# Kernel tuning notes

Measured on AMD Instinct MI355X. Metric: run time of the kernel, lower is better.

Reference implementation:

```python
import jax, jax.numpy as jnp
import numpy as np

N, FIN, H, FOUT = 4096, 128, 4, 64
NEG_INF = -1e9


def _xavier(key, shape):
    fan_in, fan_out = shape[-2], shape[-1]
    limit = float(np.sqrt(6.0 / (fan_in + fan_out)))
    return jax.random.uniform(key, shape, jnp.float32, -limit, limit)


def setup_inputs() -> dict:
    key = jax.random.key(0)
    ks = jax.random.split(key, 7)
    x = jax.random.normal(ks[0], (N, FIN), jnp.float32)
    u = jax.random.uniform(ks[1], (N, N))
    mask = jnp.where(u < 0.02, 0.0, NEG_INF).astype(jnp.float32)
    idx = jnp.arange(N)
    mask = mask.at[idx, idx].set(0.0)
    proj_param = _xavier(ks[2], (H, FIN, FOUT))          # per-head projection
    score_src = _xavier(ks[3], (H, FOUT, 1))             # scoring_fn_source (IMP1 layout)
    score_tgt = _xavier(ks[4], (H, FOUT, 1))             # scoring_fn_target
    skip_w = _xavier(ks[5], (H * FOUT, FIN))             # skip_proj Linear weight
    bias = jnp.zeros((H * FOUT,), jnp.float32)
    return {"x": x, "mask": mask, "proj_param": proj_param,
            "score_src": score_src, "score_tgt": score_tgt,
            "skip_w": skip_w, "bias": bias}


def reference(x, mask, proj_param, score_src, score_tgt, skip_w, bias):
    # project: [1,N,Fin] @ [H,Fin,Fout] -> [H,N,Fout]
    h = jnp.einsum('nf,hfo->hno', x, proj_param)
    # additive (Bahdanau-style) scores
    s_src = jnp.matmul(h, score_src)                     # [H,N,1]
    s_tgt = jnp.matmul(h, score_tgt)                     # [H,N,1]
    all_scores = jax.nn.leaky_relu(s_src + jnp.swapaxes(s_tgt, 1, 2), 0.2)  # [H,N,N]
    attn = jax.nn.softmax(all_scores + mask[None, :, :], axis=-1)           # [H,N,N]
    # aggregate: [H,N,N] @ [H,N,Fout] -> [N,H,Fout]
    out = jnp.einsum('hnm,hmo->nho', attn, h)
    # skip connection (dims differ: Fin != H*Fout -> use skip_proj)
    out = out + jnp.matmul(x, skip_w.T).reshape(N, H, FOUT)
    out = out.reshape(N, H * FOUT) + bias                # concat heads + bias
    return jax.nn.elu(out)
```

## Files before the change

kernel.cpp:

```cpp
#include <hip/hip_runtime.h>
#include <hip/hip_bf16.h>
#include <math.h>


#define NN   4096
#define FIN  128
#define NH   4
#define FO   64
#define HF   256
#define LIST 192
#define GEMM_BLOCKS 512
#define ROWS_PER 2

typedef unsigned short ushort_t;
typedef unsigned int uint4n __attribute__((ext_vector_type(4)));

__device__ __forceinline__ ushort_t f2bf(float f) {
    __hip_bfloat16 h = __float2bfloat16(f);
    union { __hip_bfloat16 h; ushort_t u; } c; c.h = h; return c.u;
}
__device__ __forceinline__ float bf2f(ushort_t u) {
    union { unsigned int i; float f; } c; c.i = ((unsigned int)u) << 16; return c.f;
}

__global__ __launch_bounds__(256) void k0_gemm(
        const float* __restrict__ x,
        const float* __restrict__ proj,
        const float* __restrict__ skw,
        const float* __restrict__ asrc,
        const float* __restrict__ atgt,
        ushort_t* __restrict__ h2b, float* __restrict__ skip_ws,
        float* __restrict__ src4, float* __restrict__ tgt4) {
    __shared__ float sA[64 * 68];
    __shared__ float sB[64 * 64];
    const int tid = threadIdx.x;
    const int blk = blockIdx.x;

    const int bc = blk >> 6;
    const int i0 = (blk & 63) * 64;
    const int tx = tid & 15, ty = tid >> 4;
    const int r0 = ty << 2, c0 = tx << 2;
    float acc[4][4] = {};

    #pragma unroll
    for (int kb = 0; kb < FIN; kb += 64) {
        if (kb) __syncthreads();
        #pragma unroll
        for (int q = 0; q < 4; q++) {
            int s   = tid + q * 256;
            int row = s >> 4;
            int c4  = (s & 15) << 2;
            float4 v = *(const float4*)(x + (size_t)(i0 + row) * FIN + kb + c4);
            float* d = sA + row * 68 + c4;
            d[0] = v.x; d[1] = v.y; d[2] = v.z; d[3] = v.w;
        }
        if (bc < 4) {
            const float4* src = (const float4*)(proj + (size_t)bc * FIN * FO
                                                + (size_t)kb * FO);
            #pragma unroll
            for (int q = 0; q < 4; q++) {
                int s = tid + q * 256;
                *(float4*)(sB + (size_t)s * 4) = src[s];
            }
        } else {
            const float* sw = skw + (size_t)(bc - 4) * 64 * FIN;
            #pragma unroll
            for (int q = 0; q < 4; q++) {
                int s  = tid + q * 256;
                int c  = s & 63;
                int k4 = (s >> 6) << 2;
                float4 v = *(const float4*)(sw + (size_t)c * FIN + kb + k4);
                sB[(k4 + 0) * 64 + c] = v.x;
                sB[(k4 + 1) * 64 + c] = v.y;
                sB[(k4 + 2) * 64 + c] = v.z;
                sB[(k4 + 3) * 64 + c] = v.w;
            }
        }
        __syncthreads();

        #pragma unroll 2
        for (int k = 0; k < 64; k += 4) {
            alignas(16) float a[4][4];
            alignas(16) float b[4][4];
            #pragma unroll
            for (int rr = 0; rr < 4; rr++)
                *(float4*)a[rr] = *(const float4*)(sA + (r0 + rr) * 68 + k);
            #pragma unroll
            for (int kk = 0; kk < 4; kk++)
                *(float4*)b[kk] = *(const float4*)(sB + (k + kk) * 64 + c0);
            #pragma unroll
            for (int kk = 0; kk < 4; kk++)
                #pragma unroll
                for (int rr = 0; rr < 4; rr++)
                    #pragma unroll
                    for (int cc = 0; cc < 4; cc++)
                        acc[rr][cc] = fmaf(a[rr][kk], b[kk][cc], acc[rr][cc]);
        }
    }

    if (bc < 4) {
        #pragma unroll
        for (int rr = 0; rr < 4; rr++) {
            ushort4 hv;
            hv.x = f2bf(acc[rr][0]); hv.y = f2bf(acc[rr][1]);
            hv.z = f2bf(acc[rr][2]); hv.w = f2bf(acc[rr][3]);
            *(ushort4*)(h2b + (size_t)(i0 + r0 + rr) * HF + bc * 64 + c0) = hv;
        }
        float as[4], at[4];
        #pragma unroll
        for (int cc = 0; cc < 4; cc++) {
            as[cc] = asrc[bc * FO + c0 + cc];
            at[cc] = atgt[bc * FO + c0 + cc];
        }
        #pragma unroll
        for (int rr = 0; rr < 4; rr++) {
            float ps = acc[rr][0] * as[0] + acc[rr][1] * as[1]
                     + acc[rr][2] * as[2] + acc[rr][3] * as[3];
            float pt = acc[rr][0] * at[0] + acc[rr][1] * at[1]
                     + acc[rr][2] * at[2] + acc[rr][3] * at[3];
            #pragma unroll
            for (int off = 8; off >= 1; off >>= 1) {
                ps += __shfl_xor(ps, off, 64);
                pt += __shfl_xor(pt, off, 64);
            }
            if (tx == 0) {
                int i = i0 + r0 + rr;
                src4[(size_t)i * 4 + bc] = ps;
                tgt4[(size_t)i * 4 + bc] = pt;
            }
        }
    } else {
        float* dst = skip_ws + (size_t)i0 * HF + (bc - 4) * 64;
        #pragma unroll
        for (int rr = 0; rr < 4; rr++)
            *(float4*)(dst + (size_t)(r0 + rr) * HF + c0) = *(float4*)acc[rr];
    }
}

struct K1Shared {
    int   s_j[LIST];
    float s_p[4][LIST + 1];
    float s_red[4][256];
    int   s_cnt[4];
    float s_inv[4];
};

__device__ __forceinline__ void k1_row(
        K1Shared* sh, unsigned hm, float sc, float skipv, float bv, int i,
        int tid, int lane, int w,
        const ushort_t* __restrict__ h2b,
        const float* __restrict__ tgt4,
        float* __restrict__ out) {
    const int cl = __popc(hm);
    int incl = cl;
    #pragma unroll
    for (int o = 1; o < 64; o <<= 1) {
        int t = __shfl_up(incl, o, 64);
        if (lane >= o) incl += t;
    }
    const int excl = incl - cl;
    if (lane == 63) sh->s_cnt[w] = incl;
    __syncthreads();
    const int t0 = sh->s_cnt[0], t1 = sh->s_cnt[1],
              t2 = sh->s_cnt[2], t3 = sh->s_cnt[3];
    const int off = (w > 0 ? t0 : 0) + (w > 1 ? t1 : 0) + (w > 2 ? t2 : 0);
    int c = t0 + t1 + t2 + t3;
    c = c < LIST ? c : LIST;

    int p = off + excl;
    unsigned mm = hm;
    while (mm) {
        int b = __builtin_ctz(mm);
        mm &= mm - 1;
        if (p < LIST)
            sh->s_j[p] = (w << 10) + ((b >> 2) << 8) + (lane << 2) + (b & 3);
        p++;
    }
    __syncthreads();

    float lsum = 0.f;
    for (int kk = lane; kk < c; kk += 64) {
        int j = sh->s_j[kk];
        float pv = sc + tgt4[(size_t)j * 4 + w];
        pv = pv > 0.f ? pv : 0.2f * pv;
        pv = __expf(pv);
        sh->s_p[w][kk] = pv;
        lsum += pv;
    }
    #pragma unroll
    for (int o = 32; o >= 1; o >>= 1)
        lsum += __shfl_xor(lsum, o, 64);
    if (lane == 0) sh->s_inv[w] = lsum > 0.f ? 1.0f / lsum : 0.0f;
    __syncthreads();

    const int h = lane >> 4;
    const ushort_t* hp = h2b + 4 * lane;
    float4 acc = {0.f, 0.f, 0.f, 0.f};
    int kk = w;
    for (; kk + 12 < c; kk += 16) {
        int   j0 = sh->s_j[kk],      j1 = sh->s_j[kk + 4];
        int   j2 = sh->s_j[kk + 8],  j3 = sh->s_j[kk + 12];
        float p0 = sh->s_p[h][kk],   p1 = sh->s_p[h][kk + 4];
        float p2 = sh->s_p[h][kk + 8], p3 = sh->s_p[h][kk + 12];
        ushort4 a0 = *(const ushort4*)(hp + (size_t)j0 * HF);
        ushort4 a1 = *(const ushort4*)(hp + (size_t)j1 * HF);
        ushort4 a2 = *(const ushort4*)(hp + (size_t)j2 * HF);
        ushort4 a3 = *(const ushort4*)(hp + (size_t)j3 * HF);
        acc.x = fmaf(p0, bf2f(a0.x), acc.x);
        acc.y = fmaf(p0, bf2f(a0.y), acc.y);
        acc.z = fmaf(p0, bf2f(a0.z), acc.z);
        acc.w = fmaf(p0, bf2f(a0.w), acc.w);
        acc.x = fmaf(p1, bf2f(a1.x), acc.x);
        acc.y = fmaf(p1, bf2f(a1.y), acc.y);
        acc.z = fmaf(p1, bf2f(a1.z), acc.z);
        acc.w = fmaf(p1, bf2f(a1.w), acc.w);
        acc.x = fmaf(p2, bf2f(a2.x), acc.x);
        acc.y = fmaf(p2, bf2f(a2.y), acc.y);
        acc.z = fmaf(p2, bf2f(a2.z), acc.z);
        acc.w = fmaf(p2, bf2f(a2.w), acc.w);
        acc.x = fmaf(p3, bf2f(a3.x), acc.x);
        acc.y = fmaf(p3, bf2f(a3.y), acc.y);
        acc.z = fmaf(p3, bf2f(a3.z), acc.z);
        acc.w = fmaf(p3, bf2f(a3.w), acc.w);
    }
    for (; kk < c; kk += 4) {
        int   j0 = sh->s_j[kk];
        float p0 = sh->s_p[h][kk];
        ushort4 a0 = *(const ushort4*)(hp + (size_t)j0 * HF);
        acc.x = fmaf(p0, bf2f(a0.x), acc.x);
        acc.y = fmaf(p0, bf2f(a0.y), acc.y);
        acc.z = fmaf(p0, bf2f(a0.z), acc.z);
        acc.w = fmaf(p0, bf2f(a0.w), acc.w);
    }
    *(float4*)&sh->s_red[w][4 * lane] = acc;
    __syncthreads();

    float tot = sh->s_red[0][tid] + sh->s_red[1][tid]
              + sh->s_red[2][tid] + sh->s_red[3][tid];
    float vv = tot * sh->s_inv[tid >> 6] + skipv + bv;
    vv = vv > 0.f ? vv : expm1f(vv);
    out[(size_t)i * HF + tid] = vv;
}

__global__ __launch_bounds__(256) void k1_attn(
        const unsigned int* __restrict__ mask,
        const ushort_t* __restrict__ h2b,
        const float* __restrict__ skip_ws,
        const float* __restrict__ src4,
        const float* __restrict__ tgt4,
        const float* __restrict__ bias,
        float* __restrict__ out) {
    __shared__ K1Shared sh;
    const int tid  = threadIdx.x;
    const int lane = tid & 63, w = tid >> 6;
    const int i0   = blockIdx.x * ROWS_PER;

    const uint4n* mb = (const uint4n*)mask;
    const size_t base = (size_t)i0 * 1024 + (size_t)(w * 256 + lane);
    uint4n m0[4];
    #pragma unroll
    for (int s = 0; s < 4; s++) m0[s] = mb[base + s * 64];

    const float skip0 = skip_ws[(size_t)i0 * HF + tid];
    const float skip1 = skip_ws[(size_t)(i0 + 1) * HF + tid];
    const float bv    = bias[tid];
    const float sc0   = src4[(size_t)i0 * 4 + w];
    const float sc1   = src4[(size_t)(i0 + 1) * 4 + w];

    unsigned hm0 = 0;
    #pragma unroll
    for (int s = 0; s < 4; s++)
        #pragma unroll
        for (int e = 0; e < 4; e++)
            hm0 |= ((m0[s][e] & 0x7fffffffu) == 0u ? 1u : 0u) << (s * 4 + e);

    uint4n m1[4];
    #pragma unroll
    for (int s = 0; s < 4; s++) m1[s] = mb[base + 1024 + s * 64];

    k1_row(&sh, hm0, sc0, skip0, bv, i0, tid, lane, w, h2b, tgt4, out);
    __syncthreads();

    unsigned hm1 = 0;
    #pragma unroll
    for (int s = 0; s < 4; s++)
        #pragma unroll
        for (int e = 0; e < 4; e++)
            hm1 |= ((m1[s][e] & 0x7fffffffu) == 0u ? 1u : 0u) << (s * 4 + e);

    k1_row(&sh, hm1, sc1, skip1, bv, i0 + 1, tid, lane, w, h2b, tgt4, out);
}

extern "C" void kernel_launch(void* const* d_in, const int* in_sizes, int n_in,
                              void* d_out, int out_size, void* d_ws, size_t ws_size,
                              hipStream_t stream) {
    const float*        x    = (const float*)d_in[0];
    const unsigned int* mask = (const unsigned int*)d_in[1];
    const float*        proj = (const float*)d_in[2];
    const float*        asrc = (const float*)d_in[3];
    const float*        atgt = (const float*)d_in[4];
    const float*        skw  = (const float*)d_in[5];
    const float*        bias = (const float*)d_in[6];
    float*              out  = (float*)d_out;

    char* ws = (char*)d_ws;
    ushort_t* h2b     = (ushort_t*)ws;
    float*    skip_ws = (float*)(ws + (2u << 20));
    float*    src4    = (float*)(ws + (6u << 20));
    float*    tgt4    = (float*)(ws + (6u << 20) + (64u << 10));

    hipLaunchKernelGGL(k0_gemm, dim3(GEMM_BLOCKS), dim3(256), 0, stream,
                       x, proj, skw, asrc, atgt,
                       h2b, skip_ws, src4, tgt4);
    hipLaunchKernelGGL(k1_attn, dim3(NN / ROWS_PER), dim3(256), 0, stream,
                       mask, h2b, skip_ws, src4, tgt4, bias, out);
}
```

Measured before the change: 128.7 us.

## Assign one wavefront per attention row and drop block-level synchronisation

Result: no change. 127.7 us (-0.8%).

```diff
diff --git a/kernel.cpp b/kernel.cpp
--- a/kernel.cpp
+++ b/kernel.cpp
@@ -10,7 +10,6 @@
 #define HF   256
 #define LIST 192
 #define GEMM_BLOCKS 512
-#define ROWS_PER 2
 
 typedef unsigned short ushort_t;
 typedef unsigned int uint4n __attribute__((ext_vector_type(4)));
@@ -137,21 +136,40 @@
     }
 }
 
-struct K1Shared {
-    int   s_j[LIST];
-    float s_p[4][LIST + 1];
-    float s_red[4][256];
-    int   s_cnt[4];
-    float s_inv[4];
-};
-
-__device__ __forceinline__ void k1_row(
-        K1Shared* sh, unsigned hm, float sc, float skipv, float bv, int i,
-        int tid, int lane, int w,
+__global__ __launch_bounds__(256, 4) void k1_attn(
+        const unsigned int* __restrict__ mask,
         const ushort_t* __restrict__ h2b,
+        const float* __restrict__ skip_ws,
+        const float* __restrict__ src4,
         const float* __restrict__ tgt4,
+        const float* __restrict__ bias,
         float* __restrict__ out) {
-    const int cl = __popc(hm);
+    __shared__ ushort_t s_j[4][LIST];
+    __shared__ uint2    s_rec[4][4][LIST + 1];
+    const int tid  = threadIdx.x;
+    const int lane = tid & 63, w = tid >> 6;
+    const int i    = blockIdx.x * 4 + w;
+    const int h    = lane >> 4;
+    const int g    = lane & 15;
+
+    const uint4n* mb = (const uint4n*)(mask + (size_t)i * NN);
+    uint4n m[16];
+    #pragma unroll
+    for (int s = 0; s < 16; s++) m[s] = mb[s * 64 + lane];
+
+    const float4 skipv = *(const float4*)(skip_ws + (size_t)i * HF + 4 * lane);
+    const float4 bv    = *(const float4*)(bias + 4 * lane);
+    const float  sc    = src4[(size_t)i * 4 + h];
+
+    unsigned long long hm = 0ull;
+    #pragma unroll
+    for (int s = 0; s < 16; s++)
+        #pragma unroll
+        for (int e = 0; e < 4; e++)
+            if ((m[s][e] & 0x7fffffffu) == 0u)
+                hm |= 1ull << (s * 4 + e);
+
+    const int cl = __popcll(hm);
     int incl = cl;
     #pragma unroll
     for (int o = 1; o < 64; o <<= 1) {
@@ -159,53 +177,52 @@
         if (lane >= o) incl += t;
     }
     const int excl = incl - cl;
-    if (lane == 63) sh->s_cnt[w] = incl;
-    __syncthreads();
-    const int t0 = sh->s_cnt[0], t1 = sh->s_cnt[1],
-              t2 = sh->s_cnt[2], t3 = sh->s_cnt[3];
-    const int off = (w > 0 ? t0 : 0) + (w > 1 ? t1 : 0) + (w > 2 ? t2 : 0);
-    int c = t0 + t1 + t2 + t3;
+    int c = __shfl(incl, 63, 64);
     c = c < LIST ? c : LIST;
 
-    int p = off + excl;
-    unsigned mm = hm;
-    while (mm) {
-        int b = __builtin_ctz(mm);
-        mm &= mm - 1;
-        if (p < LIST)
-            sh->s_j[p] = (w << 10) + ((b >> 2) << 8) + (lane << 2) + (b & 3);
-        p++;
-    }
-    __syncthreads();
+    {
+        int p = excl;
+        unsigned long long mm = hm;
+        while (mm) {
+            int b = __builtin_ctzll(mm);
+            mm &= mm - 1;
+            if (p < LIST)
+                s_j[w][p] = (ushort_t)((b >> 2) * 256 + lane * 4 + (b & 3));
+            p++;
+        }
+    }
 
     float lsum = 0.f;
-    for (int kk = lane; kk < c; kk += 64) {
-        int j = sh->s_j[kk];
-        float pv = sc + tgt4[(size_t)j * 4 + w];
+    for (int kk = g; kk < c; kk += 16) {
+        int j = s_j[w][kk];
+        float pv = sc + tgt4[(size_t)j * 4 + h];
         pv = pv > 0.f ? pv : 0.2f * pv;
         pv = __expf(pv);
-        sh->s_p[w][kk] = pv;
+        uint2 r;
+        r.x = __float_as_uint(pv);
+        r.y = (unsigned)j << 9;
+        s_rec[w][h][kk] = r;
         lsum += pv;
     }
     #pragma unroll
-    for (int o = 32; o >= 1; o >>= 1)
+    for (int o = 8; o >= 1; o >>= 1)
         lsum += __shfl_xor(lsum, o, 64);
-    if (lane == 0) sh->s_inv[w] = lsum > 0.f ? 1.0f / lsum : 0.0f;
-    __syncthreads();
-
-    const int h = lane >> 4;
-    const ushort_t* hp = h2b + 4 * lane;
+    const float inv = lsum > 0.f ? 1.0f / lsum : 0.0f;
+
+    const char* hp = (const char*)(h2b + 4 * lane);
     float4 acc = {0.f, 0.f, 0.f, 0.f};
-    int kk = w;
-    for (; kk + 12 < c; kk += 16) {
-        int   j0 = sh->s_j[kk],      j1 = sh->s_j[kk + 4];
-        int   j2 = sh->s_j[kk + 8],  j3 = sh->s_j[kk + 12];
-        float p0 = sh->s_p[h][kk],   p1 = sh->s_p[h][kk + 4];
-        float p2 = sh->s_p[h][kk + 8], p3 = sh->s_p[h][kk + 12];
-        ushort4 a0 = *(const ushort4*)(hp + (size_t)j0 * HF);
-        ushort4 a1 = *(const ushort4*)(hp + (size_t)j1 * HF);
-        ushort4 a2 = *(const ushort4*)(hp + (size_t)j2 * HF);
-        ushort4 a3 = *(const ushort4*)(hp + (size_t)j3 * HF);
+    int kk = 0;
+    for (; kk + 3 < c; kk += 4) {
+        uint2 r0 = s_rec[w][h][kk + 0];
+        uint2 r1 = s_rec[w][h][kk + 1];
+        uint2 r2 = s_rec[w][h][kk + 2];
+        uint2 r3 = s_rec[w][h][kk + 3];
+        ushort4 a0 = *(const ushort4*)(hp + r0.y);
+        ushort4 a1 = *(const ushort4*)(hp + r1.y);
+        ushort4 a2 = *(const ushort4*)(hp + r2.y);
+        ushort4 a3 = *(const ushort4*)(hp + r3.y);
+        float p0 = __uint_as_float(r0.x), p1 = __uint_as_float(r1.x);
+        float p2 = __uint_as_float(r2.x), p3 = __uint_as_float(r3.x);
         acc.x = fmaf(p0, bf2f(a0.x), acc.x);
         acc.y = fmaf(p0, bf2f(a0.y), acc.y);
         acc.z = fmaf(p0, bf2f(a0.z), acc.z);
@@ -223,72 +240,26 @@
         acc.z = fmaf(p3, bf2f(a3.z), acc.z);
         acc.w = fmaf(p3, bf2f(a3.w), acc.w);
     }
-    for (; kk < c; kk += 4) {
-        int   j0 = sh->s_j[kk];
-        float p0 = sh->s_p[h][kk];
-        ushort4 a0 = *(const ushort4*)(hp + (size_t)j0 * HF);
+    for (; kk < c; kk++) {
+        uint2 r0 = s_rec[w][h][kk];
+        ushort4 a0 = *(const ushort4*)(hp + r0.y);
+        float p0 = __uint_as_float(r0.x);
         acc.x = fmaf(p0, bf2f(a0.x), acc.x);
         acc.y = fmaf(p0, bf2f(a0.y), acc.y);
         acc.z = fmaf(p0, bf2f(a0.z), acc.z);
         acc.w = fmaf(p0, bf2f(a0.w), acc.w);
     }
-    *(float4*)&sh->s_red[w][4 * lane] = acc;
-    __syncthreads();
-
-    float tot = sh->s_red[0][tid] + sh->s_red[1][tid]
-              + sh->s_red[2][tid] + sh->s_red[3][tid];
-    float vv = tot * sh->s_inv[tid >> 6] + skipv + bv;
-    vv = vv > 0.f ? vv : expm1f(vv);
-    out[(size_t)i * HF + tid] = vv;
-}
-
-__global__ __launch_bounds__(256) void k1_attn(
-        const unsigned int* __restrict__ mask,
-        const ushort_t* __restrict__ h2b,
-        const float* __restrict__ skip_ws,
-        const float* __restrict__ src4,
-        const float* __restrict__ tgt4,
-        const float* __restrict__ bias,
-        float* __restrict__ out) {
-    __shared__ K1Shared sh;
-    const int tid  = threadIdx.x;
-    const int lane = tid & 63, w = tid >> 6;
-    const int i0   = blockIdx.x * ROWS_PER;
-
-    const uint4n* mb = (const uint4n*)mask;
-    const size_t base = (size_t)i0 * 1024 + (size_t)(w * 256 + lane);
-    uint4n m0[4];
-    #pragma unroll
-    for (int s = 0; s < 4; s++) m0[s] = mb[base + s * 64];
-
-    const float skip0 = skip_ws[(size_t)i0 * HF + tid];
-    const float skip1 = skip_ws[(size_t)(i0 + 1) * HF + tid];
-    const float bv    = bias[tid];
-    const float sc0   = src4[(size_t)i0 * 4 + w];
-    const float sc1   = src4[(size_t)(i0 + 1) * 4 + w];
-
-    unsigned hm0 = 0;
-    #pragma unroll
-    for (int s = 0; s < 4; s++)
-        #pragma unroll
-        for (int e = 0; e < 4; e++)
-            hm0 |= ((m0[s][e] & 0x7fffffffu) == 0u ? 1u : 0u) << (s * 4 + e);
-
-    uint4n m1[4];
-    #pragma unroll
-    for (int s = 0; s < 4; s++) m1[s] = mb[base + 1024 + s * 64];
-
-    k1_row(&sh, hm0, sc0, skip0, bv, i0, tid, lane, w, h2b, tgt4, out);
-    __syncthreads();
-
-    unsigned hm1 = 0;
-    #pragma unroll
-    for (int s = 0; s < 4; s++)
-        #pragma unroll
-        for (int e = 0; e < 4; e++)
-            hm1 |= ((m1[s][e] & 0x7fffffffu) == 0u ? 1u : 0u) << (s * 4 + e);
-
-    k1_row(&sh, hm1, sc1, skip1, bv, i0 + 1, tid, lane, w, h2b, tgt4, out);
+
+    float4 vv;
+    vv.x = acc.x * inv + skipv.x + bv.x;
+    vv.y = acc.y * inv + skipv.y + bv.y;
+    vv.z = acc.z * inv + skipv.z + bv.z;
+    vv.w = acc.w * inv + skipv.w + bv.w;
+    vv.x = vv.x > 0.f ? vv.x : expm1f(vv.x);
+    vv.y = vv.y > 0.f ? vv.y : expm1f(vv.y);
+    vv.z = vv.z > 0.f ? vv.z : expm1f(vv.z);
+    vv.w = vv.w > 0.f ? vv.w : expm1f(vv.w);
+    *(float4*)(out + (size_t)i * HF + 4 * lane) = vv;
 }
 
 extern "C" void kernel_launch(void* const* d_in, const int* in_sizes, int n_in,
@@ -312,6 +283,6 @@
     hipLaunchKernelGGL(k0_gemm, dim3(GEMM_BLOCKS), dim3(256), 0, stream,
                        x, proj, skw, asrc, atgt,
                        h2b, skip_ws, src4, tgt4);
-    hipLaunchKernelGGL(k1_attn, dim3(NN / ROWS_PER), dim3(256), 0, stream,
+    hipLaunchKernelGGL(k1_attn, dim3(NN / 4), dim3(256), 0, stream,
                        mask, h2b, skip_ws, src4, tgt4, bias, out);
 }
```

## Split mask scan into a separate bitmask kernel ahead of attention

Applied to the files above, without the earlier changes.

Measured after the change: 130.1 us. Within noise of the previous version (+1.0%).

```diff
diff --git a/kernel.cpp b/kernel.cpp
--- a/kernel.cpp
+++ b/kernel.cpp
@@ -10,7 +10,6 @@
 #define HF   256
 #define LIST 192
 #define GEMM_BLOCKS 512
-#define ROWS_PER 2
 
 typedef unsigned short ushort_t;
 typedef unsigned int uint4n __attribute__((ext_vector_type(4)));
@@ -137,7 +136,32 @@
     }
 }
 
-struct K1Shared {
+__global__ __launch_bounds__(256) void k_scan(
+        const unsigned int* __restrict__ mask,
+        ushort_t* __restrict__ bm) {
+    const int lane = threadIdx.x & 63, w = threadIdx.x >> 6;
+    const int wid  = blockIdx.x * 4 + w;
+    const uint4n* mb = (const uint4n*)mask;
+
+    #pragma unroll
+    for (int rep = 0; rep < 2; rep++) {
+        const int sg  = wid + rep * 8192;
+        const int row = sg >> 2, seg = sg & 3;
+        const uint4n* p = mb + (size_t)row * 1024 + seg * 256 + lane * 4;
+        uint4n v0 = p[0], v1 = p[1], v2 = p[2], v3 = p[3];
+        unsigned hm = 0;
+        #pragma unroll
+        for (int e = 0; e < 4; e++) {
+            hm |= ((v0[e] & 0x7fffffffu) == 0u ? 1u : 0u) << (0 * 4 + e);
+            hm |= ((v1[e] & 0x7fffffffu) == 0u ? 1u : 0u) << (1 * 4 + e);
+            hm |= ((v2[e] & 0x7fffffffu) == 0u ? 1u : 0u) << (2 * 4 + e);
+            hm |= ((v3[e] & 0x7fffffffu) == 0u ? 1u : 0u) << (3 * 4 + e);
+        }
+        bm[(size_t)row * 256 + seg * 64 + lane] = (ushort_t)hm;
+    }
+}
+
+struct K2Shared {
     int   s_j[LIST];
     float s_p[4][LIST + 1];
     float s_red[4][256];
@@ -145,12 +169,24 @@
     float s_inv[4];
 };
 
-__device__ __forceinline__ void k1_row(
-        K1Shared* sh, unsigned hm, float sc, float skipv, float bv, int i,
-        int tid, int lane, int w,
+__global__ __launch_bounds__(256) void k2_attn(
+        const ushort_t* __restrict__ bm,
         const ushort_t* __restrict__ h2b,
+        const float* __restrict__ skip_ws,
+        const float* __restrict__ src4,
         const float* __restrict__ tgt4,
+        const float* __restrict__ bias,
         float* __restrict__ out) {
+    __shared__ K2Shared sh;
+    const int tid  = threadIdx.x;
+    const int lane = tid & 63, w = tid >> 6;
+    const int i    = blockIdx.x;
+
+    const unsigned hm = bm[(size_t)i * 256 + w * 64 + lane];
+    const float skipv = skip_ws[(size_t)i * HF + tid];
+    const float bv    = bias[tid];
+    const float sc    = src4[(size_t)i * 4 + w];
+
     const int cl = __popc(hm);
     int incl = cl;
     #pragma unroll
@@ -159,38 +195,39 @@
         if (lane >= o) incl += t;
     }
     const int excl = incl - cl;
-    if (lane == 63) sh->s_cnt[w] = incl;
+    if (lane == 63) sh.s_cnt[w] = incl;
     __syncthreads();
-    const int t0 = sh->s_cnt[0], t1 = sh->s_cnt[1],
-              t2 = sh->s_cnt[2], t3 = sh->s_cnt[3];
+    const int t0 = sh.s_cnt[0], t1 = sh.s_cnt[1],
+              t2 = sh.s_cnt[2], t3 = sh.s_cnt[3];
     const int off = (w > 0 ? t0 : 0) + (w > 1 ? t1 : 0) + (w > 2 ? t2 : 0);
     int c = t0 + t1 + t2 + t3;
     c = c < LIST ? c : LIST;
 
-    int p = off + excl;
-    unsigned mm = hm;
-    while (mm) {
-        int b = __builtin_ctz(mm);
-        mm &= mm - 1;
-        if (p < LIST)
-            sh->s_j[p] = (w << 10) + ((b >> 2) << 8) + (lane << 2) + (b & 3);
-        p++;
+    {
+        int p = off + excl;
+        unsigned mm = hm;
+        while (mm) {
+            int b = __builtin_ctz(mm);
+            mm &= mm - 1;
+            if (p < LIST) sh.s_j[p] = (w << 10) + (lane << 4) + b;
+            p++;
+        }
     }
     __syncthreads();
 
     float lsum = 0.f;
     for (int kk = lane; kk < c; kk += 64) {
-        int j = sh->s_j[kk];
+        int j = sh.s_j[kk];
         float pv = sc + tgt4[(size_t)j * 4 + w];
         pv = pv > 0.f ? pv : 0.2f * pv;
         pv = __expf(pv);
-        sh->s_p[w][kk] = pv;
+        sh.s_p[w][kk] = pv;
         lsum += pv;
     }
     #pragma unroll
     for (int o = 32; o >= 1; o >>= 1)
         lsum += __shfl_xor(lsum, o, 64);
-    if (lane == 0) sh->s_inv[w] = lsum > 0.f ? 1.0f / lsum : 0.0f;
+    if (lane == 0) sh.s_inv[w] = lsum > 0.f ? 1.0f / lsum : 0.0f;
     __syncthreads();
 
     const int h = lane >> 4;
@@ -198,10 +235,10 @@
     float4 acc = {0.f, 0.f, 0.f, 0.f};
     int kk = w;
     for (; kk + 12 < c; kk += 16) {
-        int   j0 = sh->s_j[kk],      j1 = sh->s_j[kk + 4];
-        int   j2 = sh->s_j[kk + 8],  j3 = sh->s_j[kk + 12];
-        float p0 = sh->s_p[h][kk],   p1 = sh->s_p[h][kk + 4];
-        float p2 = sh->s_p[h][kk + 8], p3 = sh->s_p[h][kk + 12];
+        int   j0 = sh.s_j[kk],        j1 = sh.s_j[kk + 4];
+        int   j2 = sh.s_j[kk + 8],    j3 = sh.s_j[kk + 12];
+        float p0 = sh.s_p[h][kk],     p1 = sh.s_p[h][kk + 4];
+        float p2 = sh.s_p[h][kk + 8], p3 = sh.s_p[h][kk + 12];
         ushort4 a0 = *(const ushort4*)(hp + (size_t)j0 * HF);
         ushort4 a1 = *(const ushort4*)(hp + (size_t)j1 * HF);
         ushort4 a2 = *(const ushort4*)(hp + (size_t)j2 * HF);
@@ -224,71 +261,22 @@
         acc.w = fmaf(p3, bf2f(a3.w), acc.w);
     }
     for (; kk < c; kk += 4) {
-        int   j0 = sh->s_j[kk];
-        float p0 = sh->s_p[h][kk];
+        int   j0 = sh.s_j[kk];
+        float p0 = sh.s_p[h][kk];
         ushort4 a0 = *(const ushort4*)(hp + (size_t)j0 * HF);
         acc.x = fmaf(p0, bf2f(a0.x), acc.x);
         acc.y = fmaf(p0, bf2f(a0.y), acc.y);
         acc.z = fmaf(p0, bf2f(a0.z), acc.z);
         acc.w = fmaf(p0, bf2f(a0.w), acc.w);
     }
-    *(float4*)&sh->s_red[w][4 * lane] = acc;
+    *(float4*)&sh.s_red[w][4 * lane] = acc;
     __syncthreads();
 
-    float tot = sh->s_red[0][tid] + sh->s_red[1][tid]
-              + sh->s_red[2][tid] + sh->s_red[3][tid];
-    float vv = tot * sh->s_inv[tid >> 6] + skipv + bv;
+    float tot = sh.s_red[0][tid] + sh.s_red[1][tid]
+              + sh.s_red[2][tid] + sh.s_red[3][tid];
+    float vv = tot * sh.s_inv[tid >> 6] + skipv + bv;
     vv = vv > 0.f ? vv : expm1f(vv);
     out[(size_t)i * HF + tid] = vv;
-}
-
-__global__ __launch_bounds__(256) void k1_attn(
-        const unsigned int* __restrict__ mask,
-        const ushort_t* __restrict__ h2b,
-        const float* __restrict__ skip_ws,
-        const float* __restrict__ src4,
-        const float* __restrict__ tgt4,
-        const float* __restrict__ bias,
-        float* __restrict__ out) {
-    __shared__ K1Shared sh;
-    const int tid  = threadIdx.x;
-    const int lane = tid & 63, w = tid >> 6;
-    const int i0   = blockIdx.x * ROWS_PER;
-
-    const uint4n* mb = (const uint4n*)mask;
-    const size_t base = (size_t)i0 * 1024 + (size_t)(w * 256 + lane);
-    uint4n m0[4];
-    #pragma unroll
-    for (int s = 0; s < 4; s++) m0[s] = mb[base + s * 64];
-
-    const float skip0 = skip_ws[(size_t)i0 * HF + tid];
-    const float skip1 = skip_ws[(size_t)(i0 + 1) * HF + tid];
-    const float bv    = bias[tid];
-    const float sc0   = src4[(size_t)i0 * 4 + w];
-    const float sc1   = src4[(size_t)(i0 + 1) * 4 + w];
-
-    unsigned hm0 = 0;
-    #pragma unroll
-    for (int s = 0; s < 4; s++)
-        #pragma unroll
-        for (int e = 0; e < 4; e++)
-            hm0 |= ((m0[s][e] & 0x7fffffffu) == 0u ? 1u : 0u) << (s * 4 + e);
-
-    uint4n m1[4];
-    #pragma unroll
-    for (int s = 0; s < 4; s++) m1[s] = mb[base + 1024 + s * 64];
-
-    k1_row(&sh, hm0, sc0, skip0, bv, i0, tid, lane, w, h2b, tgt4, out);
-    __syncthreads();
-
-    unsigned hm1 = 0;
-    #pragma unroll
-    for (int s = 0; s < 4; s++)
-        #pragma unroll
-        for (int e = 0; e < 4; e++)
-            hm1 |= ((m1[s][e] & 0x7fffffffu) == 0u ? 1u : 0u) << (s * 4 + e);
-
-    k1_row(&sh, hm1, sc1, skip1, bv, i0 + 1, tid, lane, w, h2b, tgt4, out);
 }
 
 extern "C" void kernel_launch(void* const* d_in, const int* in_sizes, int n_in,
@@ -308,10 +296,13 @@
     float*    skip_ws = (float*)(ws + (2u << 20));
     float*    src4    = (float*)(ws + (6u << 20));
     float*    tgt4    = (float*)(ws + (6u << 20) + (64u << 10));
+    ushort_t* bm      = (ushort_t*)(ws + (8u << 20));
 
     hipLaunchKernelGGL(k0_gemm, dim3(GEMM_BLOCKS), dim3(256), 0, stream,
                        x, proj, skw, asrc, atgt,
                        h2b, skip_ws, src4, tgt4);
-    hipLaunchKernelGGL(k1_attn, dim3(NN / ROWS_PER), dim3(256), 0, stream,
-                       mask, h2b, skip_ws, src4, tgt4, bias, out);
-}
+    hipLaunchKernelGGL(k_scan, dim3(2048), dim3(256), 0, stream,
+                       mask, bm);
+    hipLaunchKernelGGL(k2_attn, dim3(NN), dim3(256), 0, stream,
+                       bm, h2b, skip_ws, src4, tgt4, bias, out);
+}
```
